# Kernel optimization log

Measured on AMD Instinct MI355X. Metric: run time of the kernel, lower is better.

Reference implementation:

```python
import jax, jax.numpy as jnp
import numpy as np

B, C, H, W = 256, 3, 84, 84
HID, VOCAB = 768, 50257
INPUT_DIM = H * W
EPS = 1e-8


def setup_inputs() -> dict:
    key = jax.random.key(0)
    k1, k2, k3 = jax.random.split(key, 3)
    observations = jax.random.normal(k1, (B, C, H, W), dtype=jnp.float32)
    word_embs = jax.random.normal(k2, (VOCAB, HID), dtype=jnp.float32)
    # torch.normal(mean=0, std=1/sqrt(hidden_dim), size=(hidden_dim, input_dim))
    rand_obs_proj = jax.random.normal(k3, (HID, INPUT_DIM), dtype=jnp.float32) / np.sqrt(HID)
    return {"observations": observations, "word_embs": word_embs,
            "rand_obs_proj": rand_obs_proj, "beta": 8}


def reference(observations, word_embs, rand_obs_proj, beta):
    # _preprocess_obs: mean over channel dim, then flatten each sample
    obs = observations.mean(axis=1).reshape(observations.shape[0], -1)  # [B, H*W]
    q = obs @ rand_obs_proj.T                                           # [B, HID]
    q_norm = jnp.linalg.norm(q, axis=-1, keepdims=True)                 # [B, 1]
    e_norm = jnp.linalg.norm(word_embs, axis=-1)[None, :]               # [1, V]
    sims = (q @ word_embs.T) / (q_norm * e_norm + EPS)                  # [B, V]
    softm = jax.nn.softmax(beta * sims, axis=-1)
    state = softm @ word_embs                                           # [B, HID]
    return state
```

## Files before the change

kernel.cpp:

```cpp
#include <hip/hip_runtime.h>


#define VOCAB 50257
#define VPAD  50304
#define HID   768
#define BATCH 256
#define IN    7056
#define INPAD 7072
#define NPAIR (INPAD / 2)
#define SPLITS 32
#define CHUNK 1600
#define QSPLITS 17
#define QCHUNK 416

typedef __attribute__((ext_vector_type(8))) __bf16 bf16x8;
typedef __attribute__((ext_vector_type(4))) float f32x4;

__device__ inline unsigned short f2bf(float f) {
  union { float f; unsigned u; } v; v.f = f;
  unsigned r = v.u + 0x7fffu + ((v.u >> 16) & 1u);
  return (unsigned short)(r >> 16);
}
__device__ inline unsigned pack2(float lo, float hi) {
  return (unsigned)f2bf(lo) | ((unsigned)f2bf(hi) << 16);
}

__global__ __launch_bounds__(256) void k_obs(const float* __restrict__ obs,
                                             unsigned* __restrict__ obsb) {
  int b = blockIdx.x, t = threadIdx.x;
  const size_t base = (size_t)b * 3 * IN;
  for (int p = t; p < NPAIR; p += 256) {
    float x = 0.f, y = 0.f;
    if (2 * p < IN) {
      float2 a0 = *(const float2*)&obs[base + 2 * p];
      float2 a1 = *(const float2*)&obs[base + IN + 2 * p];
      float2 a2 = *(const float2*)&obs[base + 2 * IN + 2 * p];
      x = (a0.x + a1.x + a2.x) * (1.f / 3.f);
      y = (a0.y + a1.y + a2.y) * (1.f / 3.f);
    }
    obsb[b * NPAIR + p] = pack2(x, y);
  }
}

__global__ __launch_bounds__(256) void k_proj(const float* __restrict__ proj,
                                              unsigned* __restrict__ projb) {
  int h = blockIdx.x, t = threadIdx.x;
  for (int p = t; p < NPAIR; p += 256) {
    float x = 0.f, y = 0.f;
    if (2 * p < IN) {
      float2 xy = *(const float2*)&proj[(size_t)h * IN + 2 * p];
      x = xy.x; y = xy.y;
    }
    projb[h * NPAIR + p] = pack2(x, y);
  }
}


__global__ __launch_bounds__(256) void k_qgemm(const unsigned short* __restrict__ A,
                                               const unsigned short* __restrict__ Bm,
                                               float* __restrict__ qp) {
  __shared__ unsigned short As[64][32];
  __shared__ unsigned short Bs[64][32];
  const int t = threadIdx.x;
  const int lane = t & 63, wave = t >> 6;
  const int wm = wave >> 1, wn = wave & 1;
  const int quad = lane >> 4, lo = lane & 15;
  const int m0 = blockIdx.y * 64, n0 = blockIdx.x * 64;
  const int split = blockIdx.z;
  const int kbeg = split * QCHUNK, kend = kbeg + QCHUNK;
  const int ar = t >> 2, ac = (t & 3) * 8;
  f32x4 acc[2][2];
  for (int i = 0; i < 2; i++)
    for (int j = 0; j < 2; j++) acc[i][j] = (f32x4){0.f, 0.f, 0.f, 0.f};
  const unsigned short* aptr = &A[(m0 + ar) * INPAD + ac];
  const unsigned short* bptr = &Bm[(n0 + ar) * INPAD + ac];
  for (int k0 = kbeg; k0 < kend; k0 += 32) {
    uint4 av = *(const uint4*)(aptr + k0);
    uint4 bv = *(const uint4*)(bptr + k0);
    __syncthreads();
    *(uint4*)&As[ar][ac] = av;
    *(uint4*)&Bs[ar][ac] = bv;
    __syncthreads();
    bf16x8 af[2], bfr[2];
    for (int i = 0; i < 2; i++) {
      af[i]  = *(const bf16x8*)&As[wm * 32 + i * 16 + lo][quad * 8];
      bfr[i] = *(const bf16x8*)&Bs[wn * 32 + i * 16 + lo][quad * 8];
    }
    for (int mi = 0; mi < 2; mi++)
      for (int ni = 0; ni < 2; ni++)
        acc[mi][ni] = __builtin_amdgcn_mfma_f32_16x16x32_bf16(af[mi], bfr[ni], acc[mi][ni], 0, 0, 0);
  }
  float* outp = qp + (size_t)split * BATCH * HID;
  for (int mi = 0; mi < 2; mi++)
    for (int ni = 0; ni < 2; ni++)
      for (int r = 0; r < 4; r++) {
        int row = m0 + wm * 32 + mi * 16 + quad * 4 + r;
        int col = n0 + wn * 32 + ni * 16 + lo;
        outp[row * HID + col] = acc[mi][ni][r];
      }
}

__global__ __launch_bounds__(384) void k_qhat(const float* __restrict__ qp,
                                              const int* __restrict__ beta,
                                              unsigned* __restrict__ qhat,
                                              float* __restrict__ l) {
  int b = blockIdx.x, t = threadIdx.x;
  float x = 0.f, y = 0.f;
  for (int s = 0; s < QSPLITS; s++) {
    float2 p = *(const float2*)&qp[(size_t)s * BATCH * HID + b * HID + 2 * t];
    x += p.x; y += p.y;
  }
  float ss = x * x + y * y;
  for (int m = 1; m < 64; m <<= 1) ss += __shfl_xor(ss, m, 64);
  __shared__ float sacc[6];
  if ((t & 63) == 0) sacc[t >> 6] = ss;
  __syncthreads();
  float tot = sacc[0] + sacc[1] + sacc[2] + sacc[3] + sacc[4] + sacc[5];
  float scale = (float)beta[0] / sqrtf(tot);
  qhat[b * (HID / 2) + t] = pack2(x * scale, y * scale);
  if (t == 0) l[b] = 0.f;
}


__global__ __launch_bounds__(256) void k_gemm1(const unsigned short* __restrict__ A,
                                               const float* __restrict__ Wf,
                                               unsigned* __restrict__ Wb,
                                               unsigned short* __restrict__ E,
                                               float* __restrict__ l) {
  __shared__ unsigned short As[128][32];
  __shared__ unsigned short Bs[128][32];
  __shared__ unsigned short Et[128][128];
  __shared__ float rowsum[128];
  __shared__ float inv_l[128];
  const int t = threadIdx.x;
  const int lane = t & 63, wave = t >> 6;
  const int wm = wave >> 1, wn = wave & 1;
  const int quad = lane >> 4, lo = lane & 15;
  const int m0 = blockIdx.x * 128, n0 = blockIdx.y * 128;
  const int ar = t >> 2, ac = (t & 3) * 8;
  const bool bx0 = (blockIdx.x == 0);
  if (t < 128) rowsum[t] = 0.f;
  f32x4 acc[4][4];
  for (int i = 0; i < 4; i++)
    for (int j = 0; j < 4; j++) acc[i][j] = (f32x4){0.f, 0.f, 0.f, 0.f};
  const unsigned short* aptr  = &A[(m0 + ar) * HID + ac];
  const unsigned short* aptr2 = &A[(m0 + ar + 64) * HID + ac];
  const int vr0 = n0 + ar, vr1 = n0 + ar + 64;
  const int vc0 = (vr0 < VOCAB) ? vr0 : (VOCAB - 1);
  const int vc1 = (vr1 < VOCAB) ? vr1 : (VOCAB - 1);
  const float* wp0 = &Wf[(size_t)vc0 * HID + ac];
  const float* wp1 = &Wf[(size_t)vc1 * HID + ac];
  float ss0 = 0.f, ss1 = 0.f;
  uint4 av0  = *(const uint4*)(aptr);
  uint4 av1  = *(const uint4*)(aptr2);
  float4 b0a = *(const float4*)(wp0);
  float4 b0b = *(const float4*)(wp0 + 4);
  float4 b1a = *(const float4*)(wp1);
  float4 b1b = *(const float4*)(wp1 + 4);
  for (int k0 = 0; k0 < HID; k0 += 32) {
    __syncthreads();
    *(uint4*)&As[ar][ac]      = av0;
    *(uint4*)&As[ar + 64][ac] = av1;
    uint4 w0 = (uint4){pack2(b0a.x, b0a.y), pack2(b0a.z, b0a.w),
                       pack2(b0b.x, b0b.y), pack2(b0b.z, b0b.w)};
    uint4 w1 = (uint4){pack2(b1a.x, b1a.y), pack2(b1a.z, b1a.w),
                       pack2(b1b.x, b1b.y), pack2(b1b.z, b1b.w)};
    *(uint4*)&Bs[ar][ac]      = w0;
    *(uint4*)&Bs[ar + 64][ac] = w1;
    ss0 += b0a.x * b0a.x + b0a.y * b0a.y + b0a.z * b0a.z + b0a.w * b0a.w
         + b0b.x * b0b.x + b0b.y * b0b.y + b0b.z * b0b.z + b0b.w * b0b.w;
    ss1 += b1a.x * b1a.x + b1a.y * b1a.y + b1a.z * b1a.z + b1a.w * b1a.w
         + b1b.x * b1b.x + b1b.y * b1b.y + b1b.z * b1b.z + b1b.w * b1b.w;
    if (bx0) {
      *(uint4*)&Wb[(size_t)vr0 * (HID / 2) + (k0 + ac) / 2] = w0;
      *(uint4*)&Wb[(size_t)vr1 * (HID / 2) + (k0 + ac) / 2] = w1;
    }
    __syncthreads();
    const int kn = (k0 + 32 < HID) ? k0 + 32 : 0;
    av0 = *(const uint4*)(aptr + kn);
    av1 = *(const uint4*)(aptr2 + kn);
    b0a = *(const float4*)(wp0 + kn);
    b0b = *(const float4*)(wp0 + kn + 4);
    b1a = *(const float4*)(wp1 + kn);
    b1b = *(const float4*)(wp1 + kn + 4);
    __builtin_amdgcn_sched_barrier(0);
    bf16x8 af[4], bfr[4];
    for (int i = 0; i < 4; i++) {
      af[i]  = *(const bf16x8*)&As[wm * 64 + i * 16 + lo][quad * 8];
      bfr[i] = *(const bf16x8*)&Bs[wn * 64 + i * 16 + lo][quad * 8];
    }
    for (int mi = 0; mi < 4; mi++)
      for (int ni = 0; ni < 4; ni++)
        acc[mi][ni] = __builtin_amdgcn_mfma_f32_16x16x32_bf16(af[mi], bfr[ni], acc[mi][ni], 0, 0, 0);
  }
  ss0 += __shfl_xor(ss0, 1, 64);
  ss0 += __shfl_xor(ss0, 2, 64);
  ss1 += __shfl_xor(ss1, 1, 64);
  ss1 += __shfl_xor(ss1, 2, 64);
  if ((t & 3) == 0) {
    inv_l[ar]      = (vr0 < VOCAB) ? (1.f / sqrtf(ss0)) : 0.f;
    inv_l[ar + 64] = (vr1 < VOCAB) ? (1.f / sqrtf(ss1)) : 0.f;
  }
  __syncthreads();
  for (int mi = 0; mi < 4; mi++)
    for (int ni = 0; ni < 4; ni++) {
      int cl = wn * 64 + ni * 16 + lo;
      int vg = n0 + cl;
      bool valid = (vg < VOCAB);
      float ie = inv_l[cl];
      for (int r = 0; r < 4; r++) {
        int row = wm * 64 + mi * 16 + quad * 4 + r;
        float e = valid ? __expf(acc[mi][ni][r] * ie) : 0.f;
        Et[row][cl] = f2bf(e);
        float s = e;
        s += __shfl_xor(s, 1, 64);
        s += __shfl_xor(s, 2, 64);
        s += __shfl_xor(s, 4, 64);
        s += __shfl_xor(s, 8, 64);
        if (lo == 0) atomicAdd(&rowsum[row], s);
      }
    }
  __syncthreads();
  for (int i = 0; i < 8; i++) {
    int idx = t + i * 256;
    int row = idx >> 4, j = idx & 15;
    *(uint4*)&E[(size_t)(m0 + row) * VPAD + n0 + j * 8] = *(const uint4*)&Et[row][j * 8];
  }
  if (t < 128) atomicAdd(&l[m0 + t], rowsum[t]);
}


__global__ __launch_bounds__(256) void k_gemm2(const unsigned short* __restrict__ Wb,
                                               const unsigned short* __restrict__ Bm,
                                               float* __restrict__ Pp) {
  __shared__ unsigned short As[128][34];
  __shared__ unsigned short Bs[128][32];
  const int t = threadIdx.x;
  const int lane = t & 63, wave = t >> 6;
  const int wm = wave >> 1, wn = wave & 1;
  const int quad = lane >> 4, lo = lane & 15;
  const int m0 = blockIdx.x * 128, n0 = blockIdx.y * 128;
  const int split = blockIdx.z;
  const int kbeg = split * CHUNK;
  const int kend = (kbeg + CHUNK < VPAD) ? kbeg + CHUNK : VPAD;
  const int sv = t >> 3, shc = t & 7;
  const int ar = t >> 2, ac = (t & 3) * 8;
  f32x4 acc[4][4];
  for (int i = 0; i < 4; i++)
    for (int j = 0; j < 4; j++) acc[i][j] = (f32x4){0.f, 0.f, 0.f, 0.f};
  const unsigned short* bptr  = &Bm[(size_t)(n0 + ar) * VPAD + ac];
  const unsigned short* bptr2 = &Bm[(size_t)(n0 + ar + 64) * VPAD + ac];
  uint4 a0  = *(const uint4*)&Wb[(size_t)(kbeg + sv) * HID + m0 + shc * 8];
  uint4 a1  = *(const uint4*)&Wb[(size_t)(kbeg + sv) * HID + m0 + (shc + 8) * 8];
  uint4 bv0 = *(const uint4*)(bptr + kbeg);
  uint4 bv1 = *(const uint4*)(bptr2 + kbeg);
  for (int k0 = kbeg; k0 < kend; k0 += 32) {
    __syncthreads();
    {
      const unsigned short* e0 = (const unsigned short*)&a0;
      const unsigned short* e1 = (const unsigned short*)&a1;
#pragma unroll
      for (int j = 0; j < 8; j++) {
        As[shc * 8 + j][sv]       = e0[j];
        As[(shc + 8) * 8 + j][sv] = e1[j];
      }
    }
    *(uint4*)&Bs[ar][ac]      = bv0;
    *(uint4*)&Bs[ar + 64][ac] = bv1;
    __syncthreads();
    const int kn = (k0 + 32 < kend) ? k0 + 32 : kbeg;
    a0  = *(const uint4*)&Wb[(size_t)(kn + sv) * HID + m0 + shc * 8];
    a1  = *(const uint4*)&Wb[(size_t)(kn + sv) * HID + m0 + (shc + 8) * 8];
    bv0 = *(const uint4*)(bptr + kn);
    bv1 = *(const uint4*)(bptr2 + kn);
    __builtin_amdgcn_sched_barrier(0);
    bf16x8 af[4], bfr[4];
#pragma unroll
    for (int i = 0; i < 4; i++) {
      const unsigned* rp = (const unsigned*)&As[wm * 64 + i * 16 + lo][quad * 8];
      uint4 u; u.x = rp[0]; u.y = rp[1]; u.z = rp[2]; u.w = rp[3];
      af[i]  = *(const bf16x8*)&u;
      bfr[i] = *(const bf16x8*)&Bs[wn * 64 + i * 16 + lo][quad * 8];
    }
    for (int mi = 0; mi < 4; mi++)
      for (int ni = 0; ni < 4; ni++)
        acc[mi][ni] = __builtin_amdgcn_mfma_f32_16x16x32_bf16(af[mi], bfr[ni], acc[mi][ni], 0, 0, 0);
  }
  float* outp = Pp + (size_t)split * HID * BATCH;
  for (int mi = 0; mi < 4; mi++)
    for (int ni = 0; ni < 4; ni++)
      for (int r = 0; r < 4; r++) {
        int h = m0 + wm * 64 + mi * 16 + quad * 4 + r;
        int b = n0 + wn * 64 + ni * 16 + lo;
        outp[h * BATCH + b] = acc[mi][ni][r];
      }
}

__global__ __launch_bounds__(256) void k_reduce(const float* __restrict__ Pp,
                                                const float* __restrict__ l,
                                                float* __restrict__ out) {
  int idx = blockIdx.x * 256 + threadIdx.x;
  int h = idx >> 8, b = idx & 255;
  float s = 0.f;
  for (int i = 0; i < SPLITS; i++) s += Pp[(size_t)i * (HID * BATCH) + idx];
  out[b * HID + h] = s / l[b];
}


extern "C" void kernel_launch(void* const* d_in, const int* in_sizes, int n_in,
                              void* d_out, int out_size, void* d_ws, size_t ws_size,
                              hipStream_t stream) {
  const float* obs  = (const float*)d_in[0];
  const float* W    = (const float*)d_in[1];
  const float* proj = (const float*)d_in[2];
  const int* beta   = (const int*)d_in[3];
  float* out = (float*)d_out;

  char* ws = (char*)d_ws;
  size_t off = 0;
  auto alloc = [&](size_t bytes) -> void* {
    void* p = ws + off;
    off = (off + bytes + 255) & ~(size_t)255;
    return p;
  };
  unsigned short* Wb    = (unsigned short*)alloc((size_t)VPAD * HID * 2);
  unsigned short* obsb  = (unsigned short*)alloc((size_t)BATCH * INPAD * 2);
  unsigned short* projb = (unsigned short*)alloc((size_t)HID * INPAD * 2);
  unsigned short* qhat  = (unsigned short*)alloc((size_t)BATCH * HID * 2);
  float* l              = (float*)alloc((size_t)BATCH * 4);
  unsigned short* E     = (unsigned short*)alloc((size_t)BATCH * VPAD * 2);
  float* Pp             = (float*)alloc((size_t)SPLITS * BATCH * HID * 4);
  float* qp             = Pp;
  (void)ws_size; (void)in_sizes; (void)n_in; (void)out_size;

  k_obs  <<<dim3(BATCH), dim3(256), 0, stream>>>(obs, (unsigned*)obsb);
  k_proj <<<dim3(HID), dim3(256), 0, stream>>>(proj, (unsigned*)projb);
  k_qgemm<<<dim3(HID / 64, BATCH / 64, QSPLITS), dim3(256), 0, stream>>>(obsb, projb, qp);
  k_qhat <<<dim3(BATCH), dim3(384), 0, stream>>>(qp, beta, (unsigned*)qhat, l);
  k_gemm1<<<dim3(BATCH / 128, VPAD / 128), dim3(256), 0, stream>>>(qhat, W, (unsigned*)Wb, E, l);
  k_gemm2<<<dim3(HID / 128, BATCH / 128, SPLITS), dim3(256), 0, stream>>>(Wb, E, Pp);
  k_reduce<<<dim3(BATCH * HID / 256), dim3(256), 0, stream>>>(Pp, l, out);
}
```

Baseline: 412.5 us.

## Drop bf16 word-embedding staging buffer; read fp32 embeddings directly in gemm2

```diff
diff --git a/kernel.cpp b/kernel.cpp
--- a/kernel.cpp
+++ b/kernel.cpp
@@ -124,12 +124,12 @@
 
 __global__ __launch_bounds__(256) void k_gemm1(const unsigned short* __restrict__ A,
                                                const float* __restrict__ Wf,
-                                               unsigned* __restrict__ Wb,
                                                unsigned short* __restrict__ E,
                                                float* __restrict__ l) {
-  __shared__ unsigned short As[128][32];
-  __shared__ unsigned short Bs[128][32];
-  __shared__ unsigned short Et[128][128];
+  __shared__ union SmemT {
+    struct { unsigned short As[128][32]; unsigned short Bs[128][32]; } k;
+    unsigned short Et[128][128];
+  } sh;
   __shared__ float rowsum[128];
   __shared__ float inv_l[128];
   const int t = threadIdx.x;
@@ -138,7 +138,6 @@
   const int quad = lane >> 4, lo = lane & 15;
   const int m0 = blockIdx.x * 128, n0 = blockIdx.y * 128;
   const int ar = t >> 2, ac = (t & 3) * 8;
-  const bool bx0 = (blockIdx.x == 0);
   if (t < 128) rowsum[t] = 0.f;
   f32x4 acc[4][4];
   for (int i = 0; i < 4; i++)
@@ -159,22 +158,18 @@
   float4 b1b = *(const float4*)(wp1 + 4);
   for (int k0 = 0; k0 < HID; k0 += 32) {
     __syncthreads();
-    *(uint4*)&As[ar][ac]      = av0;
-    *(uint4*)&As[ar + 64][ac] = av1;
+    *(uint4*)&sh.k.As[ar][ac]      = av0;
+    *(uint4*)&sh.k.As[ar + 64][ac] = av1;
     uint4 w0 = (uint4){pack2(b0a.x, b0a.y), pack2(b0a.z, b0a.w),
                        pack2(b0b.x, b0b.y), pack2(b0b.z, b0b.w)};
     uint4 w1 = (uint4){pack2(b1a.x, b1a.y), pack2(b1a.z, b1a.w),
                        pack2(b1b.x, b1b.y), pack2(b1b.z, b1b.w)};
-    *(uint4*)&Bs[ar][ac]      = w0;
-    *(uint4*)&Bs[ar + 64][ac] = w1;
+    *(uint4*)&sh.k.Bs[ar][ac]      = w0;
+    *(uint4*)&sh.k.Bs[ar + 64][ac] = w1;
     ss0 += b0a.x * b0a.x + b0a.y * b0a.y + b0a.z * b0a.z + b0a.w * b0a.w
          + b0b.x * b0b.x + b0b.y * b0b.y + b0b.z * b0b.z + b0b.w * b0b.w;
     ss1 += b1a.x * b1a.x + b1a.y * b1a.y + b1a.z * b1a.z + b1a.w * b1a.w
          + b1b.x * b1b.x + b1b.y * b1b.y + b1b.z * b1b.z + b1b.w * b1b.w;
-    if (bx0) {
-      *(uint4*)&Wb[(size_t)vr0 * (HID / 2) + (k0 + ac) / 2] = w0;
-      *(uint4*)&Wb[(size_t)vr1 * (HID / 2) + (k0 + ac) / 2] = w1;
-    }
     __syncthreads();
     const int kn = (k0 + 32 < HID) ? k0 + 32 : 0;
     av0 = *(const uint4*)(aptr + kn);
@@ -186,8 +181,8 @@
     __builtin_amdgcn_sched_barrier(0);
     bf16x8 af[4], bfr[4];
     for (int i = 0; i < 4; i++) {
-      af[i]  = *(const bf16x8*)&As[wm * 64 + i * 16 + lo][quad * 8];
-      bfr[i] = *(const bf16x8*)&Bs[wn * 64 + i * 16 + lo][quad * 8];
+      af[i]  = *(const bf16x8*)&sh.k.As[wm * 64 + i * 16 + lo][quad * 8];
+      bfr[i] = *(const bf16x8*)&sh.k.Bs[wn * 64 + i * 16 + lo][quad * 8];
     }
     for (int mi = 0; mi < 4; mi++)
       for (int ni = 0; ni < 4; ni++)
@@ -211,7 +206,7 @@
       for (int r = 0; r < 4; r++) {
         int row = wm * 64 + mi * 16 + quad * 4 + r;
         float e = valid ? __expf(acc[mi][ni][r] * ie) : 0.f;
-        Et[row][cl] = f2bf(e);
+        sh.Et[row][cl] = f2bf(e);
         float s = e;
         s += __shfl_xor(s, 1, 64);
         s += __shfl_xor(s, 2, 64);
@@ -224,13 +219,13 @@
   for (int i = 0; i < 8; i++) {
     int idx = t + i * 256;
     int row = idx >> 4, j = idx & 15;
-    *(uint4*)&E[(size_t)(m0 + row) * VPAD + n0 + j * 8] = *(const uint4*)&Et[row][j * 8];
+    *(uint4*)&E[(size_t)(m0 + row) * VPAD + n0 + j * 8] = *(const uint4*)&sh.Et[row][j * 8];
   }
   if (t < 128) atomicAdd(&l[m0 + t], rowsum[t]);
 }
 
 
-__global__ __launch_bounds__(256) void k_gemm2(const unsigned short* __restrict__ Wb,
+__global__ __launch_bounds__(256) void k_gemm2(const float* __restrict__ Wf,
                                                const unsigned short* __restrict__ Bm,
                                                float* __restrict__ Pp) {
   __shared__ unsigned short As[128][34];
@@ -245,16 +240,25 @@
   const int kend = (kbeg + CHUNK < VPAD) ? kbeg + CHUNK : VPAD;
   const int sv = t >> 3, shc = t & 7;
   const int ar = t >> 2, ac = (t & 3) * 8;
+  const int hb = m0 + shc * 8;
   f32x4 acc[4][4];
   for (int i = 0; i < 4; i++)
     for (int j = 0; j < 4; j++) acc[i][j] = (f32x4){0.f, 0.f, 0.f, 0.f};
   const unsigned short* bptr  = &Bm[(size_t)(n0 + ar) * VPAD + ac];
   const unsigned short* bptr2 = &Bm[(size_t)(n0 + ar + 64) * VPAD + ac];
-  uint4 a0  = *(const uint4*)&Wb[(size_t)(kbeg + sv) * HID + m0 + shc * 8];
-  uint4 a1  = *(const uint4*)&Wb[(size_t)(kbeg + sv) * HID + m0 + (shc + 8) * 8];
+  int vrow = kbeg + sv;
+  const float* ap = &Wf[(size_t)((vrow < VOCAB) ? vrow : (VOCAB - 1)) * HID + hb];
+  float4 a0a = *(const float4*)(ap);
+  float4 a0b = *(const float4*)(ap + 4);
+  float4 a1a = *(const float4*)(ap + 64);
+  float4 a1b = *(const float4*)(ap + 68);
   uint4 bv0 = *(const uint4*)(bptr + kbeg);
   uint4 bv1 = *(const uint4*)(bptr2 + kbeg);
   for (int k0 = kbeg; k0 < kend; k0 += 32) {
+    uint4 a0 = (uint4){pack2(a0a.x, a0a.y), pack2(a0a.z, a0a.w),
+                       pack2(a0b.x, a0b.y), pack2(a0b.z, a0b.w)};
+    uint4 a1 = (uint4){pack2(a1a.x, a1a.y), pack2(a1a.z, a1a.w),
+                       pack2(a1b.x, a1b.y), pack2(a1b.z, a1b.w)};
     __syncthreads();
     {
       const unsigned short* e0 = (const unsigned short*)&a0;
@@ -269,8 +273,12 @@
     *(uint4*)&Bs[ar + 64][ac] = bv1;
     __syncthreads();
     const int kn = (k0 + 32 < kend) ? k0 + 32 : kbeg;
-    a0  = *(const uint4*)&Wb[(size_t)(kn + sv) * HID + m0 + shc * 8];
-    a1  = *(const uint4*)&Wb[(size_t)(kn + sv) * HID + m0 + (shc + 8) * 8];
+    vrow = kn + sv;
+    ap = &Wf[(size_t)((vrow < VOCAB) ? vrow : (VOCAB - 1)) * HID + hb];
+    a0a = *(const float4*)(ap);
+    a0b = *(const float4*)(ap + 4);
+    a1a = *(const float4*)(ap + 64);
+    a1b = *(const float4*)(ap + 68);
     bv0 = *(const uint4*)(bptr + kn);
     bv1 = *(const uint4*)(bptr2 + kn);
     __builtin_amdgcn_sched_barrier(0);
@@ -323,7 +331,6 @@
     off = (off + bytes + 255) & ~(size_t)255;
     return p;
   };
-  unsigned short* Wb    = (unsigned short*)alloc((size_t)VPAD * HID * 2);
   unsigned short* obsb  = (unsigned short*)alloc((size_t)BATCH * INPAD * 2);
   unsigned short* projb = (unsigned short*)alloc((size_t)HID * INPAD * 2);
   unsigned short* qhat  = (unsigned short*)alloc((size_t)BATCH * HID * 2);
@@ -337,7 +344,7 @@
   k_proj <<<dim3(HID), dim3(256), 0, stream>>>(proj, (unsigned*)projb);
   k_qgemm<<<dim3(HID / 64, BATCH / 64, QSPLITS), dim3(256), 0, stream>>>(obsb, projb, qp);
   k_qhat <<<dim3(BATCH), dim3(384), 0, stream>>>(qp, beta, (unsigned*)qhat, l);
-  k_gemm1<<<dim3(BATCH / 128, VPAD / 128), dim3(256), 0, stream>>>(qhat, W, (unsigned*)Wb, E, l);
-  k_gemm2<<<dim3(HID / 128, BATCH / 128, SPLITS), dim3(256), 0, stream>>>(Wb, E, Pp);
+  k_gemm1<<<dim3(BATCH / 128, VPAD / 128), dim3(256), 0, stream>>>(qhat, W, E, l);
+  k_gemm2<<<dim3(HID / 128, BATCH / 128, SPLITS), dim3(256), 0, stream>>>(W, E, Pp);
   k_reduce<<<dim3(BATCH * HID / 256), dim3(256), 0, stream>>>(Pp, l, out);
 }
```

Result: no change. 412.5 us (+0.0%).
